# Kernel tuning notes

Measured on AMD Instinct MI355X. Metric: run time of the kernel, lower is better.

## Reference

```python
import jax, jax.numpy as jnp
import numpy as np

D_K = 16

def setup_inputs() -> dict:
    key = jax.random.key(0)
    kq, kk, kv, km, kb = jax.random.split(key, 5)
    B, H, S, d = 8, 16, 1024, D_K
    Q = jax.random.normal(kq, (B, H, S, d), dtype=jnp.float32)
    K = jax.random.normal(kk, (B, H, S, d), dtype=jnp.float32)
    V = jax.random.normal(kv, (B, H, S, d), dtype=jnp.float32)
    attn_mask = jax.random.randint(km, (B, 1, S, S), 0, 2).astype(jnp.bool_)
    MD_bias = jax.random.normal(kb, (B, 1, S, S), dtype=jnp.float32)
    return {"Q": Q, "K": K, "V": V, "attn_mask": attn_mask, "MD_bias": MD_bias}

def reference(Q, K, V, attn_mask, MD_bias):
    # scores: [B,H,S,S] = Q K^T / sqrt(d_k) + MD_bias, masked to -1e9
    scale = 1.0 / np.sqrt(D_K).astype(np.float32)
    scores = jnp.einsum('bhqd,bhkd->bhqk', Q, K) * scale + MD_bias
    scores = jnp.where(attn_mask, jnp.float32(-1e9), scores)
    attn = jax.nn.softmax(scores, axis=-1)
    context = jnp.einsum('bhqk,bhkd->bhqd', attn, V)
    return context
```

## Files before the change

### kernel.cpp

```cpp
#include <hip/hip_runtime.h>
#include <hip/hip_fp16.h>
#include <math.h>

#define SEQ    1024
#define DK     16
#define NHEAD  16
#define NBATCH 8
#define LOG2E  1.4426950408889634f

#define CH     128
#define NCH    (SEQ / CH)
#define KHI_STRIDE 40
#define VT_STRIDE  272
#define KHI_CH (CH * KHI_STRIDE)
#define VT_CH  (DK * VT_STRIDE)
#define BUF_SZ (KHI_CH + VT_CH)

typedef __attribute__((ext_vector_type(4))) short  short4v;
typedef __attribute__((ext_vector_type(8))) short  short8v;
typedef __attribute__((ext_vector_type(2))) short  short2v;
typedef __attribute__((ext_vector_type(4))) float  float4v;
typedef __attribute__((ext_vector_type(2))) unsigned int uint2v;

static __device__ __forceinline__ float fast_exp2(float x) {
#if __has_builtin(__builtin_amdgcn_exp2f)
    return __builtin_amdgcn_exp2f(x);
#else
    return exp2f(x);
#endif
}

static __device__ __forceinline__ float4v mfma16(short4v a, short4v b, float4v c) {
#if __has_builtin(__builtin_amdgcn_mfma_f32_16x16x16bf16_1k)
    return __builtin_amdgcn_mfma_f32_16x16x16bf16_1k(a, b, c, 0, 0, 0);
#else
    float4v d = c;
    asm volatile("v_mfma_f32_16x16x16_bf16 %0, %1, %2, %0" : "+v"(d) : "v"(a), "v"(b));
    return d;
#endif
}

static __device__ __forceinline__ float4v mfma32(short8v a, short8v b, float4v c) {
#if __has_builtin(__builtin_amdgcn_mfma_f32_16x16x32_bf16)
    return __builtin_amdgcn_mfma_f32_16x16x32_bf16(a, b, c, 0, 0, 0);
#else
    short4v a0 = {a[0], a[1], a[2], a[3]}, a1 = {a[4], a[5], a[6], a[7]};
    short4v b0 = {b[0], b[1], b[2], b[3]}, b1 = {b[4], b[5], b[6], b[7]};
    c = mfma16(a0, b0, c);
    return mfma16(a1, b1, c);
#endif
}

static __device__ __forceinline__ unsigned bf16_rne(float x) {
    unsigned u = __float_as_uint(x);
    return (u + 0x7FFFu + ((u >> 16) & 1u)) >> 16;
}
static __device__ __forceinline__ float bf16_to_f(unsigned b) {
    return __uint_as_float(b << 16);
}
static __device__ __forceinline__ unsigned pk_bf16(float a, float b) {
#if __has_builtin(__builtin_amdgcn_cvt_pk_bf16_f32)
    short2v r = __builtin_amdgcn_cvt_pk_bf16_f32(a, b);
    return __builtin_bit_cast(unsigned, r);
#else
    return bf16_rne(a) | (bf16_rne(b) << 16);
#endif
}
static __device__ __forceinline__ short4v bc_s4(unsigned lo, unsigned hi) {
    uint2v u; u.x = lo; u.y = hi;
    return __builtin_bit_cast(short4v, u);
}
static __device__ __forceinline__ unsigned h2pack(int m0, float b0, int m1, float b1) {
    const __half2 a = __floats2half2_rn(m0 ? -60000.f : b0 * LOG2E,
                                        m1 ? -60000.f : b1 * LOG2E);
    return __builtin_bit_cast(unsigned, a);
}

__global__ __launch_bounds__(256)
void prep_all(const float* __restrict__ K, const float* __restrict__ V,
              const int* __restrict__ mask, const float* __restrict__ bias,
              uint2* __restrict__ KHI, short* __restrict__ Vt,
              uint4* __restrict__ biasp) {
    const int blk = blockIdx.x;
    const int t   = threadIdx.x;
    if (blk < 2048) {
        __shared__ uint4 BsT[64][9];
        const int b    = blk >> 8;
        const int qt64 = (blk >> 4) & 15;
        const int c    = (blk >> 1) & 7;
        const int half = blk & 1;
        const int kb   = c * 128 + half * 64;
        #pragma unroll
        for (int i = 0; i < 4; ++i) {
            const int idx = t + i * 256;
            const int row = idx >> 4;
            const int c4  = idx & 15;
            const size_t ga = ((size_t)b * SEQ + qt64 * 64 + row) * SEQ + kb + c4 * 4;
            const float4 bv = *(const float4*)(bias + ga);
            const int4   mv = *(const int4*)(mask + ga);
            uint2 u;
            u.x = h2pack(mv.x, bv.x, mv.y, bv.y);
            u.y = h2pack(mv.z, bv.z, mv.w, bv.w);
            const int jj = c4 >> 1;
            ((uint2*)&BsT[row][jj ^ (row & 7)])[c4 & 1] = u;
        }
        __syncthreads();
        const int w = t >> 6, lane = t & 63, n = lane & 15, g = lane >> 4;
        const int row = w * 16 + n;
        #pragma unroll
        for (int tpl = 0; tpl < 2; ++tpl) {
            const int tp = half * 2 + tpl;
            const int jj = tpl * 4 + g;
            const uint4 v = BsT[row][jj ^ (row & 7)];
            const size_t ob = ((((size_t)(b * 16 + qt64) * 4 + w) * 8 + c) * 4 + tp) * 64 + lane;
            biasp[ob] = v;
        }
    } else if (blk < 2560) {
        const int base = (blk - 2048) * 1024;
        #pragma unroll
        for (int i = 0; i < 4; ++i) {
            const int i4 = base + t + i * 256;
            const float4 k = ((const float4*)K)[i4];
            uint2 o;
            o.x = pk_bf16(k.x, k.y);
            o.y = pk_bf16(k.z, k.w);
            KHI[i4] = o;
        }
    } else {
        __shared__ float Vs[64][17];
        const int vb = blk - 2560;
        const int bh = vb >> 2;
        const int qq = vb & 3;
        #pragma unroll
        for (int st = 0; st < 4; ++st) {
            const int s0 = qq * 256 + st * 64;
            {
                const int row = t >> 2, c4 = t & 3;
                const float4 v = ((const float4*)V)[((size_t)bh * SEQ + s0 + row) * 4 + c4];
                Vs[row][c4 * 4 + 0] = v.x; Vs[row][c4 * 4 + 1] = v.y;
                Vs[row][c4 * 4 + 2] = v.z; Vs[row][c4 * 4 + 3] = v.w;
            }
            __syncthreads();
            const int d = t >> 4, sg = t & 15;
            short4v o;
            #pragma unroll
            for (int i = 0; i < 4; ++i) o[i] = (short)bf16_rne(Vs[sg * 4 + i][d]);
            ((short4v*)Vt)[(((size_t)bh * DK + d) * SEQ + s0) / 4 + sg] = o;
            __syncthreads();
        }
    }
}

__global__ __launch_bounds__(256, 4)
void sdpa_flash(const float* __restrict__ Q, const uint2* __restrict__ KHI,
                const short* __restrict__ Vt, const uint4* __restrict__ biasp,
                float* __restrict__ out) {
    __shared__ __align__(16) char smem[2][BUF_SZ];

    const int tid  = threadIdx.x;
    const int wave = tid >> 6;
    const int lane = tid & 63;
    const int n    = lane & 15;
    const int g    = lane >> 4;
    const int permn = ((n >> 2) << 3) | (n & 3);

    const int b  = blockIdx.x & 7;
    const int j  = blockIdx.x >> 3;
    const int qt = j & 7;
    const int h  = j >> 3;
    const int q0 = qt * 128;

    const size_t bh = (size_t)b * NHEAD + h;

    short4v qh[2], ql[2];
    size_t  bfbase[2];
    #pragma unroll
    for (int f = 0; f < 2; ++f) {
        const int qrow = q0 + f * 64 + wave * 16 + n;
        const float4 qv = *(const float4*)(Q + (bh * SEQ + qrow) * DK + g * 4);
        const float qsc = 0.25f * LOG2E;
        const float v[4] = {qv.x * qsc, qv.y * qsc, qv.z * qsc, qv.w * qsc};
        #pragma unroll
        for (int e = 0; e < 4; ++e) {
            const unsigned hu = bf16_rne(v[e]);
            qh[f][e] = (short)hu;
            ql[f][e] = (short)bf16_rne(v[e] - bf16_to_f(hu));
        }
        bfbase[f] = (((size_t)(b * 16 + qt * 2 + f) * 4 + wave) * 32) * 64 + lane;
    }

    const uint4* KHIh = (const uint4*)(KHI + bh * SEQ * 4);
    const uint4* VtH  = (const uint4*)(Vt + bh * DK * SEQ);

    float4v acc[2], accl[2];
    acc[0]  = (float4v){0.f, 0.f, 0.f, 0.f};
    acc[1]  = (float4v){0.f, 0.f, 0.f, 0.f};
    accl[0] = (float4v){0.f, 0.f, 0.f, 0.f};
    accl[1] = (float4v){0.f, 0.f, 0.f, 0.f};
    const short8v ones8 = {(short)0x3F80, (short)0x3F80, (short)0x3F80, (short)0x3F80,
                           (short)0x3F80, (short)0x3F80, (short)0x3F80, (short)0x3F80};

    uint4 st0, st2;
    {
        st0 = KHIh[tid];
        st2 = VtH[(tid >> 4) * 128 + (tid & 15)];
        char* s = smem[0];
        *(uint4*)(s + (tid >> 1) * KHI_STRIDE + (tid & 1) * 16) = st0;
        *(uint4*)(s + KHI_CH + (tid >> 4) * VT_STRIDE + (tid & 15) * 16) = st2;
    }
    __syncthreads();

    for (int c = 0; c < NCH; ++c) {
        const int cur = c & 1;
        if (c < NCH - 1) {
            st0 = KHIh[(c + 1) * 256 + tid];
            st2 = VtH[(tid >> 4) * 128 + (c + 1) * 16 + (tid & 15)];
        }
        uint4 bb[2][4];
        #pragma unroll
        for (int f = 0; f < 2; ++f)
            #pragma unroll
            for (int tp = 0; tp < 4; ++tp)
                bb[f][tp] = biasp[bfbase[f] + (size_t)(c * 4 + tp) * 64];

        const char* khl = smem[cur];
        const char* vtl = smem[cur] + KHI_CH;

        #pragma unroll
        for (int tp = 0; tp < 4; ++tp) {
            const int rowA = tp * 32 + permn;
            const uint2 kAu = *(const uint2*)(khl + rowA * KHI_STRIDE + g * 8);
            const uint2 kBu = *(const uint2*)(khl + (rowA + 4) * KHI_STRIDE + g * 8);
            const uint4 vv  = *(const uint4*)(vtl + n * VT_STRIDE + tp * 64 + g * 16);
            const short4v khiA = bc_s4(kAu.x, kAu.y);
            const short4v khiB = bc_s4(kBu.x, kBu.y);
            const short8v vt8  = __builtin_bit_cast(short8v, vv);

            #pragma unroll
            for (int f = 0; f < 2; ++f) {
                const float2 a01 = __half22float2(__builtin_bit_cast(__half2, bb[f][tp].x));
                const float2 a23 = __half22float2(__builtin_bit_cast(__half2, bb[f][tp].y));
                float4v sA; sA[0] = a01.x; sA[1] = a01.y; sA[2] = a23.x; sA[3] = a23.y;
                sA = mfma16(khiA, qh[f], sA);
                sA = mfma16(khiA, ql[f], sA);
                const float2 b01 = __half22float2(__builtin_bit_cast(__half2, bb[f][tp].z));
                const float2 b23 = __half22float2(__builtin_bit_cast(__half2, bb[f][tp].w));
                float4v sB; sB[0] = b01.x; sB[1] = b01.y; sB[2] = b23.x; sB[3] = b23.y;
                sB = mfma16(khiB, qh[f], sB);
                sB = mfma16(khiB, ql[f], sB);

                const float pA0 = fast_exp2(sA[0]), pA1 = fast_exp2(sA[1]);
                const float pA2 = fast_exp2(sA[2]), pA3 = fast_exp2(sA[3]);
                const float pB0 = fast_exp2(sB[0]), pB1 = fast_exp2(sB[1]);
                const float pB2 = fast_exp2(sB[2]), pB3 = fast_exp2(sB[3]);

                uint4 pu;
                pu.x = pk_bf16(pA0, pA1);
                pu.y = pk_bf16(pA2, pA3);
                pu.z = pk_bf16(pB0, pB1);
                pu.w = pk_bf16(pB2, pB3);
                const short8v pf8 = __builtin_bit_cast(short8v, pu);

                acc[f]  = mfma32(pf8, vt8,  acc[f]);
                accl[f] = mfma32(pf8, ones8, accl[f]);
            }
        }

        if (c < NCH - 1) {
            char* s = smem[cur ^ 1];
            *(uint4*)(s + (tid >> 1) * KHI_STRIDE + (tid & 1) * 16) = st0;
            *(uint4*)(s + KHI_CH + (tid >> 4) * VT_STRIDE + (tid & 15) * 16) = st2;
        }
        __syncthreads();
    }

    #pragma unroll
    for (int f = 0; f < 2; ++f) {
        const size_t obase = bh * SEQ + q0 + f * 64 + wave * 16;
        #pragma unroll
        for (int r = 0; r < 4; ++r) {
            out[(obase + 4 * g + r) * DK + n] = acc[f][r] / accl[f][r];
        }
    }
}

#define FTQ 256
#define FTK 32
__global__ __launch_bounds__(256, 2)
void sdpa_fallback(const float* __restrict__ Q, const float* __restrict__ K,
                   const float* __restrict__ V, const int* __restrict__ mask,
                   const float* __restrict__ bias, float* __restrict__ out) {
    __shared__ float Ks[FTK][DK];
    __shared__ float Vs[FTK][DK];
    __shared__ float Bsf[FTQ][FTK + 1];

    const int tid = threadIdx.x;
    const int blk = blockIdx.x;
    const int h   = blk & (NHEAD - 1);
    const int qt  = (blk >> 4) & 3;
    const int b   = blk >> 6;
    const int q0  = qt * FTQ;
    const float qscale = 0.25f * LOG2E;
    const size_t bh = (size_t)b * NHEAD + h;

    float Qr[DK];
    {
        const float4* q4 = (const float4*)(Q + (bh * SEQ + q0 + tid) * DK);
        #pragma unroll
        for (int i = 0; i < 4; ++i) {
            float4 v = q4[i];
            Qr[4*i+0] = v.x * qscale; Qr[4*i+1] = v.y * qscale;
            Qr[4*i+2] = v.z * qscale; Qr[4*i+3] = v.w * qscale;
        }
    }
    float acc[DK];
    #pragma unroll
    for (int d = 0; d < DK; ++d) acc[d] = 0.0f;
    float l = 0.0f;

    const float* Kbase = K + bh * SEQ * DK;
    const float* Vbase = V + bh * SEQ * DK;
    const float* Bbase = bias + ((size_t)b * SEQ + q0) * SEQ;
    const int*   Mbase = mask + ((size_t)b * SEQ + q0) * SEQ;

    for (int t = 0; t < SEQ / FTK; ++t) {
        const int k0 = t * FTK;
        if (tid < 128) {
            float4 kv = ((const float4*)(Kbase + (size_t)k0 * DK))[tid];
            float4 vv = ((const float4*)(Vbase + (size_t)k0 * DK))[tid];
            ((float4*)&Ks[0][0])[tid] = kv;
            ((float4*)&Vs[0][0])[tid] = vv;
        }
        #pragma unroll
        for (int i = 0; i < 8; ++i) {
            int e4 = tid + i * 256, row = e4 >> 3, c4 = e4 & 7;
            const float4 bv = *(const float4*)(Bbase + (size_t)row * SEQ + k0 + c4 * 4);
            const int4   mv = *(const int4*)  (Mbase + (size_t)row * SEQ + k0 + c4 * 4);
            float* dst = &Bsf[row][c4 * 4];
            dst[0] = mv.x ? -1e9f : bv.x * LOG2E;
            dst[1] = mv.y ? -1e9f : bv.y * LOG2E;
            dst[2] = mv.z ? -1e9f : bv.z * LOG2E;
            dst[3] = mv.w ? -1e9f : bv.w * LOG2E;
        }
        __syncthreads();
        #pragma unroll 4
        for (int kk = 0; kk < FTK; ++kk) {
            float s = Bsf[tid][kk];
            const float4 k0v = *(const float4*)&Ks[kk][0];
            const float4 k1v = *(const float4*)&Ks[kk][4];
            const float4 k2v = *(const float4*)&Ks[kk][8];
            const float4 k3v = *(const float4*)&Ks[kk][12];
            s = fmaf(Qr[0],  k0v.x, s); s = fmaf(Qr[1],  k0v.y, s);
            s = fmaf(Qr[2],  k0v.z, s); s = fmaf(Qr[3],  k0v.w, s);
            s = fmaf(Qr[4],  k1v.x, s); s = fmaf(Qr[5],  k1v.y, s);
            s = fmaf(Qr[6],  k1v.z, s); s = fmaf(Qr[7],  k1v.w, s);
            s = fmaf(Qr[8],  k2v.x, s); s = fmaf(Qr[9],  k2v.y, s);
            s = fmaf(Qr[10], k2v.z, s); s = fmaf(Qr[11], k2v.w, s);
            s = fmaf(Qr[12], k3v.x, s); s = fmaf(Qr[13], k3v.y, s);
            s = fmaf(Qr[14], k3v.z, s); s = fmaf(Qr[15], k3v.w, s);
            float p = fast_exp2(s);
            l += p;
            const float4 v0 = *(const float4*)&Vs[kk][0];
            const float4 v1 = *(const float4*)&Vs[kk][4];
            const float4 v2 = *(const float4*)&Vs[kk][8];
            const float4 v3 = *(const float4*)&Vs[kk][12];
            acc[0]  = fmaf(p, v0.x, acc[0]);  acc[1]  = fmaf(p, v0.y, acc[1]);
            acc[2]  = fmaf(p, v0.z, acc[2]);  acc[3]  = fmaf(p, v0.w, acc[3]);
            acc[4]  = fmaf(p, v1.x, acc[4]);  acc[5]  = fmaf(p, v1.y, acc[5]);
            acc[6]  = fmaf(p, v1.z, acc[6]);  acc[7]  = fmaf(p, v1.w, acc[7]);
            acc[8]  = fmaf(p, v2.x, acc[8]);  acc[9]  = fmaf(p, v2.y, acc[9]);
            acc[10] = fmaf(p, v2.z, acc[10]); acc[11] = fmaf(p, v2.w, acc[11]);
            acc[12] = fmaf(p, v3.x, acc[12]); acc[13] = fmaf(p, v3.y, acc[13]);
            acc[14] = fmaf(p, v3.z, acc[14]); acc[15] = fmaf(p, v3.w, acc[15]);
        }
        __syncthreads();
    }
    const float inv = 1.0f / l;
    float4* o4 = (float4*)(out + (bh * SEQ + q0 + tid) * DK);
    #pragma unroll
    for (int i = 0; i < 4; ++i) {
        float4 v;
        v.x = acc[4*i+0] * inv; v.y = acc[4*i+1] * inv;
        v.z = acc[4*i+2] * inv; v.w = acc[4*i+3] * inv;
        o4[i] = v;
    }
}

extern "C" void kernel_launch(void* const* d_in, const int* in_sizes, int n_in,
                              void* d_out, int out_size, void* d_ws, size_t ws_size,
                              hipStream_t stream) {
    const float* Q    = (const float*)d_in[0];
    const float* K    = (const float*)d_in[1];
    const float* V    = (const float*)d_in[2];
    const int*   mask = (const int*)  d_in[3];
    const float* bias = (const float*)d_in[4];
    float* out = (float*)d_out;

    const size_t nKeys    = (size_t)NBATCH * NHEAD * SEQ;
    const size_t khiBytes = nKeys * 32;
    const size_t vtBytes  = nKeys * DK * sizeof(short);
    const size_t bpBytes  = (size_t)NBATCH * SEQ * SEQ * 2;
    const size_t need     = khiBytes + vtBytes + bpBytes;

    if (ws_size >= need) {
        char* w = (char*)d_ws;
        uint2* KHI   = (uint2*)(w);
        short* Vt    = (short*)(w + khiBytes);
        uint4* biasp = (uint4*)(w + khiBytes + vtBytes);

        prep_all<<<3072, 256, 0, stream>>>(K, V, mask, bias, KHI, Vt, biasp);
        sdpa_flash<<<1024, 256, 0, stream>>>(Q, KHI, Vt, biasp, out);
    } else {
        sdpa_fallback<<<NBATCH * NHEAD * (SEQ / FTQ), FTQ, 0, stream>>>(Q, K, V, mask, bias, out);
    }
}
```

Before: 155.2 us.

## Fuse preprocessing into flash kernel, reading raw bias/mask/K/V directly

Removes the separate prep kernel that packed bias+mask into fp16, converted K to bf16 and transposed V. The attention kernel now reads fp32 bias and int mask straight from global memory and converts K/V to bf16 while staging into shared memory. Block ordering is changed so the 16 heads of a batch and query tile run adjacently, letting them share the bias/mask rows through L2. This saves a launch and the workspace round trip, at the cost of each block reading the full-size fp32 bias and int32 mask (4x the packed bytes) out of cache.

```diff
diff --git a/kernel.cpp b/kernel.cpp
--- a/kernel.cpp
+++ b/kernel.cpp
@@ -1,5 +1,4 @@
 #include <hip/hip_runtime.h>
-#include <hip/hip_fp16.h>
 #include <math.h>
 
 #define SEQ    1024
@@ -7,6 +6,7 @@
 #define NHEAD  16
 #define NBATCH 8
 #define LOG2E  1.4426950408889634f
+#define NEGBIG -60000.0f
 
 #define CH     128
 #define NCH    (SEQ / CH)
@@ -70,91 +70,11 @@
     uint2v u; u.x = lo; u.y = hi;
     return __builtin_bit_cast(short4v, u);
 }
-static __device__ __forceinline__ unsigned h2pack(int m0, float b0, int m1, float b1) {
-    const __half2 a = __floats2half2_rn(m0 ? -60000.f : b0 * LOG2E,
-                                        m1 ? -60000.f : b1 * LOG2E);
-    return __builtin_bit_cast(unsigned, a);
-}
-
-__global__ __launch_bounds__(256)
-void prep_all(const float* __restrict__ K, const float* __restrict__ V,
-              const int* __restrict__ mask, const float* __restrict__ bias,
-              uint2* __restrict__ KHI, short* __restrict__ Vt,
-              uint4* __restrict__ biasp) {
-    const int blk = blockIdx.x;
-    const int t   = threadIdx.x;
-    if (blk < 2048) {
-        __shared__ uint4 BsT[64][9];
-        const int b    = blk >> 8;
-        const int qt64 = (blk >> 4) & 15;
-        const int c    = (blk >> 1) & 7;
-        const int half = blk & 1;
-        const int kb   = c * 128 + half * 64;
-        #pragma unroll
-        for (int i = 0; i < 4; ++i) {
-            const int idx = t + i * 256;
-            const int row = idx >> 4;
-            const int c4  = idx & 15;
-            const size_t ga = ((size_t)b * SEQ + qt64 * 64 + row) * SEQ + kb + c4 * 4;
-            const float4 bv = *(const float4*)(bias + ga);
-            const int4   mv = *(const int4*)(mask + ga);
-            uint2 u;
-            u.x = h2pack(mv.x, bv.x, mv.y, bv.y);
-            u.y = h2pack(mv.z, bv.z, mv.w, bv.w);
-            const int jj = c4 >> 1;
-            ((uint2*)&BsT[row][jj ^ (row & 7)])[c4 & 1] = u;
-        }
-        __syncthreads();
-        const int w = t >> 6, lane = t & 63, n = lane & 15, g = lane >> 4;
-        const int row = w * 16 + n;
-        #pragma unroll
-        for (int tpl = 0; tpl < 2; ++tpl) {
-            const int tp = half * 2 + tpl;
-            const int jj = tpl * 4 + g;
-            const uint4 v = BsT[row][jj ^ (row & 7)];
-            const size_t ob = ((((size_t)(b * 16 + qt64) * 4 + w) * 8 + c) * 4 + tp) * 64 + lane;
-            biasp[ob] = v;
-        }
-    } else if (blk < 2560) {
-        const int base = (blk - 2048) * 1024;
-        #pragma unroll
-        for (int i = 0; i < 4; ++i) {
-            const int i4 = base + t + i * 256;
-            const float4 k = ((const float4*)K)[i4];
-            uint2 o;
-            o.x = pk_bf16(k.x, k.y);
-            o.y = pk_bf16(k.z, k.w);
-            KHI[i4] = o;
-        }
-    } else {
-        __shared__ float Vs[64][17];
-        const int vb = blk - 2560;
-        const int bh = vb >> 2;
-        const int qq = vb & 3;
-        #pragma unroll
-        for (int st = 0; st < 4; ++st) {
-            const int s0 = qq * 256 + st * 64;
-            {
-                const int row = t >> 2, c4 = t & 3;
-                const float4 v = ((const float4*)V)[((size_t)bh * SEQ + s0 + row) * 4 + c4];
-                Vs[row][c4 * 4 + 0] = v.x; Vs[row][c4 * 4 + 1] = v.y;
-                Vs[row][c4 * 4 + 2] = v.z; Vs[row][c4 * 4 + 3] = v.w;
-            }
-            __syncthreads();
-            const int d = t >> 4, sg = t & 15;
-            short4v o;
-            #pragma unroll
-            for (int i = 0; i < 4; ++i) o[i] = (short)bf16_rne(Vs[sg * 4 + i][d]);
-            ((short4v*)Vt)[(((size_t)bh * DK + d) * SEQ + s0) / 4 + sg] = o;
-            __syncthreads();
-        }
-    }
-}
 
 __global__ __launch_bounds__(256, 4)
-void sdpa_flash(const float* __restrict__ Q, const uint2* __restrict__ KHI,
-                const short* __restrict__ Vt, const uint4* __restrict__ biasp,
-                float* __restrict__ out) {
+void sdpa_fused(const float* __restrict__ Q, const float* __restrict__ K,
+                const float* __restrict__ V, const int* __restrict__ mask,
+                const float* __restrict__ bias, float* __restrict__ out) {
     __shared__ __align__(16) char smem[2][BUF_SZ];
 
     const int tid  = threadIdx.x;
@@ -166,14 +86,15 @@
 
     const int b  = blockIdx.x & 7;
     const int j  = blockIdx.x >> 3;
-    const int qt = j & 7;
-    const int h  = j >> 3;
+    const int h  = j & 15;
+    const int qt = j >> 4;
     const int q0 = qt * 128;
 
     const size_t bh = (size_t)b * NHEAD + h;
 
     short4v qh[2], ql[2];
-    size_t  bfbase[2];
+    const float* bRow[2];
+    const int*   mRow[2];
     #pragma unroll
     for (int f = 0; f < 2; ++f) {
         const int qrow = q0 + f * 64 + wave * 16 + n;
@@ -186,11 +107,16 @@
             qh[f][e] = (short)hu;
             ql[f][e] = (short)bf16_rne(v[e] - bf16_to_f(hu));
         }
-        bfbase[f] = (((size_t)(b * 16 + qt * 2 + f) * 4 + wave) * 32) * 64 + lane;
-    }
-
-    const uint4* KHIh = (const uint4*)(KHI + bh * SEQ * 4);
-    const uint4* VtH  = (const uint4*)(Vt + bh * DK * SEQ);
+        const size_t roff = ((size_t)b * SEQ + qrow) * (size_t)SEQ;
+        bRow[f] = bias + roff;
+        mRow[f] = mask + roff;
+    }
+
+    const float* Kb = K + bh * SEQ * DK;
+    const float* Vb = V + bh * SEQ * DK;
+
+    const int skey = tid >> 1, shh = tid & 1;
+    const int sk2  = tid >> 2, sdq = tid & 3;
 
     float4v acc[2], accl[2];
     acc[0]  = (float4v){0.f, 0.f, 0.f, 0.f};
@@ -200,28 +126,40 @@
     const short8v ones8 = {(short)0x3F80, (short)0x3F80, (short)0x3F80, (short)0x3F80,
                            (short)0x3F80, (short)0x3F80, (short)0x3F80, (short)0x3F80};
 
-    uint4 st0, st2;
+    float4 ka0, ka1, va0, va1;
+
+    auto stage_write = [&](char* s) {
+        uint4 kp;
+        kp.x = pk_bf16(ka0.x, ka0.y); kp.y = pk_bf16(ka0.z, ka0.w);
+        kp.z = pk_bf16(ka1.x, ka1.y); kp.w = pk_bf16(ka1.z, ka1.w);
+        *(uint4*)(s + skey * KHI_STRIDE + shh * 16) = kp;
+        char* sv = s + KHI_CH;
+        const float* pa = (const float*)&va0;
+        const float* pb = (const float*)&va1;
+        #pragma unroll
+        for (int jj = 0; jj < 4; ++jj)
+            *(unsigned*)(sv + (4 * sdq + jj) * VT_STRIDE + sk2 * 4) =
+                pk_bf16(pa[jj], pb[jj]);
+    };
+
     {
-        st0 = KHIh[tid];
-        st2 = VtH[(tid >> 4) * 128 + (tid & 15)];
-        char* s = smem[0];
-        *(uint4*)(s + (tid >> 1) * KHI_STRIDE + (tid & 1) * 16) = st0;
-        *(uint4*)(s + KHI_CH + (tid >> 4) * VT_STRIDE + (tid & 15) * 16) = st2;
+        ka0 = *(const float4*)(Kb + skey * DK + shh * 8);
+        ka1 = *(const float4*)(Kb + skey * DK + shh * 8 + 4);
+        va0 = *(const float4*)(Vb + (2 * sk2) * DK + sdq * 4);
+        va1 = *(const float4*)(Vb + (2 * sk2 + 1) * DK + sdq * 4);
+        stage_write(smem[0]);
     }
     __syncthreads();
 
     for (int c = 0; c < NCH; ++c) {
         const int cur = c & 1;
         if (c < NCH - 1) {
-            st0 = KHIh[(c + 1) * 256 + tid];
-            st2 = VtH[(tid >> 4) * 128 + (c + 1) * 16 + (tid & 15)];
-        }
-        uint4 bb[2][4];
-        #pragma unroll
-        for (int f = 0; f < 2; ++f)
-            #pragma unroll
-            for (int tp = 0; tp < 4; ++tp)
-                bb[f][tp] = biasp[bfbase[f] + (size_t)(c * 4 + tp) * 64];
+            const int kc = (c + 1) * CH;
+            ka0 = *(const float4*)(Kb + (kc + skey) * DK + shh * 8);
+            ka1 = *(const float4*)(Kb + (kc + skey) * DK + shh * 8 + 4);
+            va0 = *(const float4*)(Vb + (kc + 2 * sk2) * DK + sdq * 4);
+            va1 = *(const float4*)(Vb + (kc + 2 * sk2 + 1) * DK + sdq * 4);
+        }
 
         const char* khl = smem[cur];
         const char* vtl = smem[cur] + KHI_CH;
@@ -235,17 +173,27 @@
             const short4v khiA = bc_s4(kAu.x, kAu.y);
             const short4v khiB = bc_s4(kBu.x, kBu.y);
             const short8v vt8  = __builtin_bit_cast(short8v, vv);
+            const int kk = c * CH + tp * 32 + 8 * g;
 
             #pragma unroll
             for (int f = 0; f < 2; ++f) {
-                const float2 a01 = __half22float2(__builtin_bit_cast(__half2, bb[f][tp].x));
-                const float2 a23 = __half22float2(__builtin_bit_cast(__half2, bb[f][tp].y));
-                float4v sA; sA[0] = a01.x; sA[1] = a01.y; sA[2] = a23.x; sA[3] = a23.y;
+                const float4 bA = *(const float4*)(bRow[f] + kk);
+                const float4 bB = *(const float4*)(bRow[f] + kk + 4);
+                const int4   mA = *(const int4*)  (mRow[f] + kk);
+                const int4   mB = *(const int4*)  (mRow[f] + kk + 4);
+
+                float4v sA;
+                sA[0] = mA.x ? NEGBIG : bA.x * LOG2E;
+                sA[1] = mA.y ? NEGBIG : bA.y * LOG2E;
+                sA[2] = mA.z ? NEGBIG : bA.z * LOG2E;
+                sA[3] = mA.w ? NEGBIG : bA.w * LOG2E;
                 sA = mfma16(khiA, qh[f], sA);
                 sA = mfma16(khiA, ql[f], sA);
-                const float2 b01 = __half22float2(__builtin_bit_cast(__half2, bb[f][tp].z));
-                const float2 b23 = __half22float2(__builtin_bit_cast(__half2, bb[f][tp].w));
-                float4v sB; sB[0] = b01.x; sB[1] = b01.y; sB[2] = b23.x; sB[3] = b23.y;
+                float4v sB;
+                sB[0] = mB.x ? NEGBIG : bB.x * LOG2E;
+                sB[1] = mB.y ? NEGBIG : bB.y * LOG2E;
+                sB[2] = mB.z ? NEGBIG : bB.z * LOG2E;
+                sB[3] = mB.w ? NEGBIG : bB.w * LOG2E;
                 sB = mfma16(khiB, qh[f], sB);
                 sB = mfma16(khiB, ql[f], sB);
 
@@ -266,11 +214,7 @@
             }
         }
 
-        if (c < NCH - 1) {
-            char* s = smem[cur ^ 1];
-            *(uint4*)(s + (tid >> 1) * KHI_STRIDE + (tid & 1) * 16) = st0;
-            *(uint4*)(s + KHI_CH + (tid >> 4) * VT_STRIDE + (tid & 15) * 16) = st2;
-        }
+        if (c < NCH - 1) stage_write(smem[cur ^ 1]);
         __syncthreads();
     }
 
@@ -284,111 +228,10 @@
     }
 }
 
-#define FTQ 256
-#define FTK 32
-__global__ __launch_bounds__(256, 2)
-void sdpa_fallback(const float* __restrict__ Q, const float* __restrict__ K,
-                   const float* __restrict__ V, const int* __restrict__ mask,
-                   const float* __restrict__ bias, float* __restrict__ out) {
-    __shared__ float Ks[FTK][DK];
-    __shared__ float Vs[FTK][DK];
-    __shared__ float Bsf[FTQ][FTK + 1];
-
-    const int tid = threadIdx.x;
-    const int blk = blockIdx.x;
-    const int h   = blk & (NHEAD - 1);
-    const int qt  = (blk >> 4) & 3;
-    const int b   = blk >> 6;
-    const int q0  = qt * FTQ;
-    const float qscale = 0.25f * LOG2E;
-    const size_t bh = (size_t)b * NHEAD + h;
-
-    float Qr[DK];
-    {
-        const float4* q4 = (const float4*)(Q + (bh * SEQ + q0 + tid) * DK);
-        #pragma unroll
-        for (int i = 0; i < 4; ++i) {
-            float4 v = q4[i];
-            Qr[4*i+0] = v.x * qscale; Qr[4*i+1] = v.y * qscale;
-            Qr[4*i+2] = v.z * qscale; Qr[4*i+3] = v.w * qscale;
-        }
-    }
-    float acc[DK];
-    #pragma unroll
-    for (int d = 0; d < DK; ++d) acc[d] = 0.0f;
-    float l = 0.0f;
-
-    const float* Kbase = K + bh * SEQ * DK;
-    const float* Vbase = V + bh * SEQ * DK;
-    const float* Bbase = bias + ((size_t)b * SEQ + q0) * SEQ;
-    const int*   Mbase = mask + ((size_t)b * SEQ + q0) * SEQ;
-
-    for (int t = 0; t < SEQ / FTK; ++t) {
-        const int k0 = t * FTK;
-        if (tid < 128) {
-            float4 kv = ((const float4*)(Kbase + (size_t)k0 * DK))[tid];
-            float4 vv = ((const float4*)(Vbase + (size_t)k0 * DK))[tid];
-            ((float4*)&Ks[0][0])[tid] = kv;
-            ((float4*)&Vs[0][0])[tid] = vv;
-        }
-        #pragma unroll
-        for (int i = 0; i < 8; ++i) {
-            int e4 = tid + i * 256, row = e4 >> 3, c4 = e4 & 7;
-            const float4 bv = *(const float4*)(Bbase + (size_t)row * SEQ + k0 + c4 * 4);
-            const int4   mv = *(const int4*)  (Mbase + (size_t)row * SEQ + k0 + c4 * 4);
-            float* dst = &Bsf[row][c4 * 4];
-            dst[0] = mv.x ? -1e9f : bv.x * LOG2E;
-            dst[1] = mv.y ? -1e9f : bv.y * LOG2E;
-            dst[2] = mv.z ? -1e9f : bv.z * LOG2E;
-            dst[3] = mv.w ? -1e9f : bv.w * LOG2E;
-        }
-        __syncthreads();
-        #pragma unroll 4
-        for (int kk = 0; kk < FTK; ++kk) {
-            float s = Bsf[tid][kk];
-            const float4 k0v = *(const float4*)&Ks[kk][0];
-            const float4 k1v = *(const float4*)&Ks[kk][4];
-            const float4 k2v = *(const float4*)&Ks[kk][8];
-            const float4 k3v = *(const float4*)&Ks[kk][12];
-            s = fmaf(Qr[0],  k0v.x, s); s = fmaf(Qr[1],  k0v.y, s);
-            s = fmaf(Qr[2],  k0v.z, s); s = fmaf(Qr[3],  k0v.w, s);
-            s = fmaf(Qr[4],  k1v.x, s); s = fmaf(Qr[5],  k1v.y, s);
-            s = fmaf(Qr[6],  k1v.z, s); s = fmaf(Qr[7],  k1v.w, s);
-            s = fmaf(Qr[8],  k2v.x, s); s = fmaf(Qr[9],  k2v.y, s);
-            s = fmaf(Qr[10], k2v.z, s); s = fmaf(Qr[11], k2v.w, s);
-            s = fmaf(Qr[12], k3v.x, s); s = fmaf(Qr[13], k3v.y, s);
-            s = fmaf(Qr[14], k3v.z, s); s = fmaf(Qr[15], k3v.w, s);
-            float p = fast_exp2(s);
-            l += p;
-            const float4 v0 = *(const float4*)&Vs[kk][0];
-            const float4 v1 = *(const float4*)&Vs[kk][4];
-            const float4 v2 = *(const float4*)&Vs[kk][8];
-            const float4 v3 = *(const float4*)&Vs[kk][12];
-            acc[0]  = fmaf(p, v0.x, acc[0]);  acc[1]  = fmaf(p, v0.y, acc[1]);
-            acc[2]  = fmaf(p, v0.z, acc[2]);  acc[3]  = fmaf(p, v0.w, acc[3]);
-            acc[4]  = fmaf(p, v1.x, acc[4]);  acc[5]  = fmaf(p, v1.y, acc[5]);
-            acc[6]  = fmaf(p, v1.z, acc[6]);  acc[7]  = fmaf(p, v1.w, acc[7]);
-            acc[8]  = fmaf(p, v2.x, acc[8]);  acc[9]  = fmaf(p, v2.y, acc[9]);
-            acc[10] = fmaf(p, v2.z, acc[10]); acc[11] = fmaf(p, v2.w, acc[11]);
-            acc[12] = fmaf(p, v3.x, acc[12]); acc[13] = fmaf(p, v3.y, acc[13]);
-            acc[14] = fmaf(p, v3.z, acc[14]); acc[15] = fmaf(p, v3.w, acc[15]);
-        }
-        __syncthreads();
-    }
-    const float inv = 1.0f / l;
-    float4* o4 = (float4*)(out + (bh * SEQ + q0 + tid) * DK);
-    #pragma unroll
-    for (int i = 0; i < 4; ++i) {
-        float4 v;
-        v.x = acc[4*i+0] * inv; v.y = acc[4*i+1] * inv;
-        v.z = acc[4*i+2] * inv; v.w = acc[4*i+3] * inv;
-        o4[i] = v;
-    }
-}
-
 extern "C" void kernel_launch(void* const* d_in, const int* in_sizes, int n_in,
                               void* d_out, int out_size, void* d_ws, size_t ws_size,
                               hipStream_t stream) {
+    (void)in_sizes; (void)n_in; (void)out_size; (void)d_ws; (void)ws_size;
     const float* Q    = (const float*)d_in[0];
     const float* K    = (const float*)d_in[1];
     const float* V    = (const float*)d_in[2];
@@ -396,21 +239,5 @@
     const float* bias = (const float*)d_in[4];
     float* out = (float*)d_out;
 
-    const size_t nKeys    = (size_t)NBATCH * NHEAD * SEQ;
-    const size_t khiBytes = nKeys * 32;
-    const size_t vtBytes  = nKeys * DK * sizeof(short);
-    const size_t bpBytes  = (size_t)NBATCH * SEQ * SEQ * 2;
-    const size_t need     = khiBytes + vtBytes + bpBytes;
-
-    if (ws_size >= need) {
-        char* w = (char*)d_ws;
-        uint2* KHI   = (uint2*)(w);
-        short* Vt    = (short*)(w + khiBytes);
-        uint4* biasp = (uint4*)(w + khiBytes + vtBytes);
-
-        prep_all<<<3072, 256, 0, stream>>>(K, V, mask, bias, KHI, Vt, biasp);
-        sdpa_flash<<<1024, 256, 0, stream>>>(Q, KHI, Vt, biasp, out);
-    } else {
-        sdpa_fallback<<<NBATCH * NHEAD * (SEQ / FTQ), FTQ, 0, stream>>>(Q, K, V, mask, bias, out);
-    }
-}
+    sdpa_fused<<<NBATCH * NHEAD * (SEQ / 128), 256, 0, stream>>>(Q, K, V, mask, bias, out);
+}
```

New measurement: 227.8 us. +46.8%, slower.

## Halve query tile per block to 64 rows, doubling grid and occupancy

Applied to the files above, without the earlier changes.

Each flash block now processes 64 query rows instead of 128, with one fragment per wave instead of two, and the grid doubles to 2048 blocks. Launch bounds are raised to 8 blocks per SIMD-group target, cutting register use. This aims for more parallelism and latency hiding. The cost is that each K/V chunk staged in shared memory is reused by half as many queries, doubling K/V global and LDS traffic.

```diff
diff --git a/kernel.cpp b/kernel.cpp
--- a/kernel.cpp
+++ b/kernel.cpp
@@ -151,7 +151,7 @@
     }
 }
 
-__global__ __launch_bounds__(256, 4)
+__global__ __launch_bounds__(256, 8)
 void sdpa_flash(const float* __restrict__ Q, const uint2* __restrict__ KHI,
                 const short* __restrict__ Vt, const uint4* __restrict__ biasp,
                 float* __restrict__ out) {
@@ -164,39 +164,35 @@
     const int g    = lane >> 4;
     const int permn = ((n >> 2) << 3) | (n & 3);
 
-    const int b  = blockIdx.x & 7;
-    const int j  = blockIdx.x >> 3;
-    const int qt = j & 7;
-    const int h  = j >> 3;
-    const int q0 = qt * 128;
+    const int b    = blockIdx.x & 7;
+    const int j    = blockIdx.x >> 3;
+    const int qt64 = j & 15;
+    const int h    = j >> 4;
+    const int q0   = qt64 * 64;
 
     const size_t bh = (size_t)b * NHEAD + h;
 
-    short4v qh[2], ql[2];
-    size_t  bfbase[2];
-    #pragma unroll
-    for (int f = 0; f < 2; ++f) {
-        const int qrow = q0 + f * 64 + wave * 16 + n;
+    short4v qh, ql;
+    {
+        const int qrow = q0 + wave * 16 + n;
         const float4 qv = *(const float4*)(Q + (bh * SEQ + qrow) * DK + g * 4);
         const float qsc = 0.25f * LOG2E;
         const float v[4] = {qv.x * qsc, qv.y * qsc, qv.z * qsc, qv.w * qsc};
         #pragma unroll
         for (int e = 0; e < 4; ++e) {
             const unsigned hu = bf16_rne(v[e]);
-            qh[f][e] = (short)hu;
-            ql[f][e] = (short)bf16_rne(v[e] - bf16_to_f(hu));
-        }
-        bfbase[f] = (((size_t)(b * 16 + qt * 2 + f) * 4 + wave) * 32) * 64 + lane;
-    }
+            qh[e] = (short)hu;
+            ql[e] = (short)bf16_rne(v[e] - bf16_to_f(hu));
+        }
+    }
+    const size_t bfbase = (((size_t)(b * 16 + qt64) * 4 + wave) * 32) * 64 + lane;
 
     const uint4* KHIh = (const uint4*)(KHI + bh * SEQ * 4);
     const uint4* VtH  = (const uint4*)(Vt + bh * DK * SEQ);
 
-    float4v acc[2], accl[2];
-    acc[0]  = (float4v){0.f, 0.f, 0.f, 0.f};
-    acc[1]  = (float4v){0.f, 0.f, 0.f, 0.f};
-    accl[0] = (float4v){0.f, 0.f, 0.f, 0.f};
-    accl[1] = (float4v){0.f, 0.f, 0.f, 0.f};
+    float4v acc, accl;
+    acc  = (float4v){0.f, 0.f, 0.f, 0.f};
+    accl = (float4v){0.f, 0.f, 0.f, 0.f};
     const short8v ones8 = {(short)0x3F80, (short)0x3F80, (short)0x3F80, (short)0x3F80,
                            (short)0x3F80, (short)0x3F80, (short)0x3F80, (short)0x3F80};
 
@@ -216,12 +212,10 @@
             st0 = KHIh[(c + 1) * 256 + tid];
             st2 = VtH[(tid >> 4) * 128 + (c + 1) * 16 + (tid & 15)];
         }
-        uint4 bb[2][4];
-        #pragma unroll
-        for (int f = 0; f < 2; ++f)
-            #pragma unroll
-            for (int tp = 0; tp < 4; ++tp)
-                bb[f][tp] = biasp[bfbase[f] + (size_t)(c * 4 + tp) * 64];
+        uint4 bb[4];
+        #pragma unroll
+        for (int tp = 0; tp < 4; ++tp)
+            bb[tp] = biasp[bfbase + (size_t)(c * 4 + tp) * 64];
 
         const char* khl = smem[cur];
         const char* vtl = smem[cur] + KHI_CH;
@@ -236,34 +230,31 @@
             const short4v khiB = bc_s4(kBu.x, kBu.y);
             const short8v vt8  = __builtin_bit_cast(short8v, vv);
 
-            #pragma unroll
-            for (int f = 0; f < 2; ++f) {
-                const float2 a01 = __half22float2(__builtin_bit_cast(__half2, bb[f][tp].x));
-                const float2 a23 = __half22float2(__builtin_bit_cast(__half2, bb[f][tp].y));
-                float4v sA; sA[0] = a01.x; sA[1] = a01.y; sA[2] = a23.x; sA[3] = a23.y;
-                sA = mfma16(khiA, qh[f], sA);
-                sA = mfma16(khiA, ql[f], sA);
-                const float2 b01 = __half22float2(__builtin_bit_cast(__half2, bb[f][tp].z));
-                const float2 b23 = __half22float2(__builtin_bit_cast(__half2, bb[f][tp].w));
-                float4v sB; sB[0] = b01.x; sB[1] = b01.y; sB[2] = b23.x; sB[3] = b23.y;
-                sB = mfma16(khiB, qh[f], sB);
-                sB = mfma16(khiB, ql[f], sB);
-
-                const float pA0 = fast_exp2(sA[0]), pA1 = fast_exp2(sA[1]);
-                const float pA2 = fast_exp2(sA[2]), pA3 = fast_exp2(sA[3]);
-                const float pB0 = fast_exp2(sB[0]), pB1 = fast_exp2(sB[1]);
-                const float pB2 = fast_exp2(sB[2]), pB3 = fast_exp2(sB[3]);
-
-                uint4 pu;
-                pu.x = pk_bf16(pA0, pA1);
-                pu.y = pk_bf16(pA2, pA3);
-                pu.z = pk_bf16(pB0, pB1);
-                pu.w = pk_bf16(pB2, pB3);
-                const short8v pf8 = __builtin_bit_cast(short8v, pu);
-
-                acc[f]  = mfma32(pf8, vt8,  acc[f]);
-                accl[f] = mfma32(pf8, ones8, accl[f]);
-            }
+            const float2 a01 = __half22float2(__builtin_bit_cast(__half2, bb[tp].x));
+            const float2 a23 = __half22float2(__builtin_bit_cast(__half2, bb[tp].y));
+            float4v sA; sA[0] = a01.x; sA[1] = a01.y; sA[2] = a23.x; sA[3] = a23.y;
+            sA = mfma16(khiA, qh, sA);
+            sA = mfma16(khiA, ql, sA);
+            const float2 b01 = __half22float2(__builtin_bit_cast(__half2, bb[tp].z));
+            const float2 b23 = __half22float2(__builtin_bit_cast(__half2, bb[tp].w));
+            float4v sB; sB[0] = b01.x; sB[1] = b01.y; sB[2] = b23.x; sB[3] = b23.y;
+            sB = mfma16(khiB, qh, sB);
+            sB = mfma16(khiB, ql, sB);
+
+            const float pA0 = fast_exp2(sA[0]), pA1 = fast_exp2(sA[1]);
+            const float pA2 = fast_exp2(sA[2]), pA3 = fast_exp2(sA[3]);
+            const float pB0 = fast_exp2(sB[0]), pB1 = fast_exp2(sB[1]);
+            const float pB2 = fast_exp2(sB[2]), pB3 = fast_exp2(sB[3]);
+
+            uint4 pu;
+            pu.x = pk_bf16(pA0, pA1);
+            pu.y = pk_bf16(pA2, pA3);
+            pu.z = pk_bf16(pB0, pB1);
+            pu.w = pk_bf16(pB2, pB3);
+            const short8v pf8 = __builtin_bit_cast(short8v, pu);
+
+            acc  = mfma32(pf8, vt8,  acc);
+            accl = mfma32(pf8, ones8, accl);
         }
 
         if (c < NCH - 1) {
@@ -274,12 +265,11 @@
         __syncthreads();
     }
 
-    #pragma unroll
-    for (int f = 0; f < 2; ++f) {
-        const size_t obase = bh * SEQ + q0 + f * 64 + wave * 16;
+    {
+        const size_t obase = bh * SEQ + q0 + wave * 16;
         #pragma unroll
         for (int r = 0; r < 4; ++r) {
-            out[(obase + 4 * g + r) * DK + n] = acc[f][r] / accl[f][r];
+            out[(obase + 4 * g + r) * DK + n] = acc[r] / accl[r];
         }
     }
 }
@@ -409,7 +399,7 @@
         uint4* biasp = (uint4*)(w + khiBytes + vtBytes);
 
         prep_all<<<3072, 256, 0, stream>>>(K, V, mask, bias, KHI, Vt, biasp);
-        sdpa_flash<<<1024, 256, 0, stream>>>(Q, KHI, Vt, biasp, out);
+        sdpa_flash<<<NBATCH * NHEAD * (SEQ / 64), 256, 0, stream>>>(Q, KHI, Vt, biasp, out);
     } else {
         sdpa_fallback<<<NBATCH * NHEAD * (SEQ / FTQ), FTQ, 0, stream>>>(Q, K, V, mask, bias, out);
     }
```

Result: slower. 165.4 us (+6.6%).
